# Optimization experiments

Hardware: AMD Instinct MI355X
Metric: run time of the kernel (lower is better)

## Reference

```python
import jax, jax.numpy as jnp
import numpy as np

LOG2 = np.float32(np.log(2.0))

def ssp(v):
    # shifted softplus used by SchNet
    return jax.nn.softplus(v) - LOG2

def setup_inputs() -> dict:
    key = jax.random.key(0)
    ks = jax.random.split(key, 12)
    B, A, T = 2, 512, 512          # batch, atoms, triplet-neighbors
    n_in, n_f, n_out, n_rbf = 128, 128, 128, 25
    x = jax.random.normal(ks[0], (B, A, n_in), dtype=jnp.float32)
    r_ij = jax.random.uniform(ks[1], (B, A, T, n_rbf), dtype=jnp.float32)
    pairwise_mask = jnp.ones((B, A, T), dtype=jnp.float32)
    neighbors_j = jax.random.randint(ks[2], (B, A, T), 0, A)
    neighbors_k = jax.random.randint(ks[3], (B, A, T), 0, A)
    s = 1.0 / np.sqrt(n_f)
    Wf1 = jax.random.normal(ks[4], (n_rbf, n_f), dtype=jnp.float32) / np.sqrt(n_rbf)
    bf1 = jnp.zeros((n_f,), dtype=jnp.float32)
    Wf2 = jax.random.normal(ks[5], (n_f, n_f), dtype=jnp.float32) * s
    bf2 = jnp.zeros((n_f,), dtype=jnp.float32)
    Win = jax.random.normal(ks[6], (n_in, n_f), dtype=jnp.float32) / np.sqrt(n_in)
    Wout = jax.random.normal(ks[7], (n_f, n_out), dtype=jnp.float32) * s
    bout = jnp.zeros((n_out,), dtype=jnp.float32)
    return {"x": x, "r_ij": r_ij, "pairwise_mask": pairwise_mask,
            "Wf1": Wf1, "bf1": bf1, "Wf2": Wf2, "bf2": bf2,
            "Win": Win, "Wout": Wout, "bout": bout,
            "neighbors_j": neighbors_j, "neighbors_k": neighbors_k}

def reference(x, r_ij, pairwise_mask, Wf1, bf1, Wf2, bf2, Win, Wout, bout,
              neighbors_j, neighbors_k):
    # filter network: Dense(n_rbf,F, ssp) -> Dense(F,F)
    W = ssp(jnp.einsum('batr,rf->batf', r_ij, Wf1) + bf1)
    W = jnp.einsum('batf,fg->batg', W, Wf2) + bf2          # [B,A,T,F]
    # in2f (no bias)
    y = jnp.einsum('bai,if->baf', x, Win)                  # [B,A,F]
    # double gather over triplet indices j,k (per-batch gather on atom axis)
    gather = jax.vmap(lambda yb, idx: yb[idx])             # [A,F],[A,T]->[A,T,F]
    y_j = gather(y, neighbors_j)                           # [B,A,T,F]
    y_k = gather(y, neighbors_k)                           # [B,A,T,F]
    # triple product + masked sum over triplet axis
    y = jnp.sum(y_j * W * y_k * pairwise_mask[..., None], axis=2)  # [B,A,F]
    # f2out with shifted-softplus activation
    return ssp(jnp.einsum('baf,fo->bao', y, Wout) + bout)
```

## Files before the change

### kernel.cpp

```cpp
#include <hip/hip_runtime.h>
#include <hip/hip_bf16.h>

typedef unsigned short u16;
typedef __attribute__((ext_vector_type(8))) short short8;
typedef __bf16 bf16x8 __attribute__((ext_vector_type(8)));
typedef __attribute__((ext_vector_type(4))) float float4v;
typedef __attribute__((ext_vector_type(4))) int int4v;

#define BB 2
#define AA 512
#define TT 512
#define FF 128
#define NRBF 25

__device__ float g_y[BB * AA * FF];
__device__ int   g_dtype;


__device__ __forceinline__ float bf2f(u16 u) {
    unsigned int v = ((unsigned int)u) << 16;
    return __builtin_bit_cast(float, v);
}
__device__ __forceinline__ u16 f2bf(float f) {
    unsigned int u = __builtin_bit_cast(unsigned int, f);
    u += 0x7fffu + ((u >> 16) & 1u);
    return (u16)(u >> 16);
}
__device__ __forceinline__ void split2(float v, u16& h, u16& l) {
    h = f2bf(v);
    l = f2bf(v - bf2f(h));
}
template<bool F32>
__device__ __forceinline__ float loadf(const void* p, int i) {
    return F32 ? ((const float*)p)[i] : bf2f(((const u16*)p)[i]);
}
__device__ __forceinline__ float ssp(float v) {
    float a = fabsf(v);
    float e = __builtin_amdgcn_exp2f(a * -1.44269504088896f);
    float l = __builtin_amdgcn_logf(1.0f + e);
    return fmaxf(v, 0.0f) + fmaf(0.69314718055995f, l, -0.69314718055995f);
}
__device__ __forceinline__ float4v mfma16(short8 a, short8 b, float4v c) {
    return __builtin_amdgcn_mfma_f32_16x16x32_bf16(
        __builtin_bit_cast(bf16x8, a), __builtin_bit_cast(bf16x8, b), c, 0, 0, 0);
}

__global__ __launch_bounds__(64) void k_detect(const void* r_raw) {
    const u16* p = (const u16*)r_raw;
    const int l = threadIdx.x;
    int sign = 0, zeros = 0;
#pragma unroll
    for (int i = 0; i < 8; ++i) {
        u16 v = p[2 * (l * 8 + i)];
        sign  += (v >> 15);
        zeros += (v == 0);
    }
#pragma unroll
    for (int off = 1; off < 64; off <<= 1) {
        sign  += __shfl_xor(sign, off);
        zeros += __shfl_xor(zeros, off);
    }
    if (l == 0) g_dtype = (sign || zeros > 400) ? 1 : 0;
}

template<bool F32>
__global__ __launch_bounds__(128) void k_in2f(const void* __restrict__ x,
                                              const void* __restrict__ Win) {
    if (g_dtype != (F32 ? 1 : 0)) return;
    int ba = blockIdx.x;
    int o  = threadIdx.x;
    __shared__ float sx[FF];
    sx[o] = loadf<F32>(x, ba * FF + o);
    __syncthreads();
    float s = 0.f;
#pragma unroll 8
    for (int i = 0; i < FF; ++i)
        s = fmaf(sx[i], loadf<F32>(Win, i * FF + o), s);
    g_y[ba * FF + o] = s;
}

template<bool F32>
__global__ __launch_bounds__(256, 3) void k_main(
    const void* __restrict__ r_ij, const void* __restrict__ mask,
    const void* __restrict__ Wf1,  const void* __restrict__ bf1,
    const void* __restrict__ Wf2,  const void* __restrict__ bf2_,
    const void* __restrict__ Wout, const void* __restrict__ bout,
    const int* __restrict__ nbrj,  const int* __restrict__ nbrk,
    void* __restrict__ out)
{
    if (g_dtype != (F32 ? 1 : 0)) return;
    const int ba  = blockIdx.x;
    const int tid = threadIdx.x;
    const int w   = tid >> 6;
    const int l   = tid & 63;
    const int lm  = l & 15;
    const int lq  = l >> 4;

    __shared__ __align__(16) u16 sRh[2][16][40];
    __shared__ __align__(16) u16 sRl[2][16][40];
    __shared__ __align__(16) u16 sH1h[16][136];
    __shared__ __align__(16) u16 sH1l[16][136];
    __shared__ __align__(16) int   sJ[2][16];
    __shared__ __align__(16) int   sK[2][16];
    __shared__ __align__(16) float sM[2][16];
    __shared__ float sAcc[FF];

    short8 fWf1h[2], fWf1l[2];
    short8 fWf2h[4][2], fWf2l[4][2];
    float  bf1v[2], bf2v[2];
#pragma unroll
    for (int q = 0; q < 2; ++q) {
        const int n = 32 * w + 16 * q + lm;
        short8 vh, vl;
#pragma unroll
        for (int j = 0; j < 8; ++j) {
            const int k = lq * 8 + j;
            float wv = (k < NRBF) ? loadf<F32>(Wf1, k * FF + n) : 0.f;
            u16 h, lo; split2(wv, h, lo);
            vh[j] = (short)h; vl[j] = (short)lo;
        }
        fWf1h[q] = vh;
        if (F32) fWf1l[q] = vl;
        bf1v[q] = loadf<F32>(bf1, n);
        bf2v[q] = loadf<F32>(bf2_, n);
#pragma unroll
        for (int kk = 0; kk < 4; ++kk) {
            short8 uh, ul;
#pragma unroll
            for (int j = 0; j < 8; ++j) {
                float wv = loadf<F32>(Wf2, (kk * 32 + lq * 8 + j) * FF + n);
                u16 h, lo; split2(wv, h, lo);
                uh[j] = (short)h; ul[j] = (short)lo;
            }
            fWf2h[kk][q] = uh;
            if (F32) fWf2l[kk][q] = ul;
        }
    }

    const float* yb = g_y + (ba >> 9) * (AA * FF);
    const float4v zero = {0.f, 0.f, 0.f, 0.f};
    float acc[2] = {0.f, 0.f};

    const int tt0 = tid >> 5,          k0 = tid & 31;
    const int tt1 = (tid + 256) >> 5,  k1 = tid & 31;

    {
        float v0 = (k0 < NRBF) ? loadf<F32>(r_ij, (ba * TT + tt0) * NRBF + k0) : 0.f;
        float v1 = (k1 < NRBF) ? loadf<F32>(r_ij, (ba * TT + tt1) * NRBF + k1) : 0.f;
        u16 h, lo;
        split2(v0, h, lo); sRh[0][tt0][k0] = h; if (F32) sRl[0][tt0][k0] = lo;
        split2(v1, h, lo); sRh[0][tt1][k1] = h; if (F32) sRl[0][tt1][k1] = lo;
        if (tid < 16) {
            sJ[0][tid] = nbrj[ba * TT + tid] & (AA - 1);
            sK[0][tid] = nbrk[ba * TT + tid] & (AA - 1);
            sM[0][tid] = loadf<F32>(mask, ba * TT + tid);
        }
    }

    for (int tile = 0; tile < TT / 16; ++tile) {
        const int b = tile & 1;
        __syncthreads();

        const int4v  Jv = *(const int4v*) &sJ[b][lq * 4];
        const int4v  Kv = *(const int4v*) &sK[b][lq * 4];
        const float4v Mv = *(const float4v*)&sM[b][lq * 4];
        float yjr[2][4], ykr[2][4];
#pragma unroll
        for (int q = 0; q < 2; ++q) {
            const int n = 32 * w + 16 * q + lm;
#pragma unroll
            for (int r = 0; r < 4; ++r) {
                yjr[q][r] = yb[Jv[r] * FF + n];
                ykr[q][r] = yb[Kv[r] * FF + n];
            }
        }

        float pre0 = 0.f, pre1 = 0.f, preM = 0.f;
        int   preJ = 0,   preK = 0;
        if (tile + 1 < TT / 16) {
            const int t0n = (tile + 1) * 16;
            if (k0 < NRBF)
                pre0 = loadf<F32>(r_ij, (ba * TT + t0n + tt0) * NRBF + k0);
            if (k1 < NRBF)
                pre1 = loadf<F32>(r_ij, (ba * TT + t0n + tt1) * NRBF + k1);
            if (tid < 16) {
                preJ = nbrj[ba * TT + t0n + tid];
                preK = nbrk[ba * TT + t0n + tid];
                preM = loadf<F32>(mask, ba * TT + t0n + tid);
            }
        }

        short8 aRh = *(const short8*)((const char*)&sRh[b][0][0] + lm * 80 + lq * 16);
        float4v c1[2];
        c1[0] = mfma16(aRh, fWf1h[0], zero);
        c1[1] = mfma16(aRh, fWf1h[1], zero);
        if (F32) {
            short8 aRl = *(const short8*)((const char*)&sRl[b][0][0] + lm * 80 + lq * 16);
            c1[0] = mfma16(aRl, fWf1h[0], c1[0]);
            c1[1] = mfma16(aRl, fWf1h[1], c1[1]);
            c1[0] = mfma16(aRh, fWf1l[0], c1[0]);
            c1[1] = mfma16(aRh, fWf1l[1], c1[1]);
        }
#pragma unroll
        for (int q = 0; q < 2; ++q) {
            const int n = 32 * w + 16 * q + lm;
#pragma unroll
            for (int r = 0; r < 4; ++r) {
                const int m = lq * 4 + r;
                float h1 = ssp(c1[q][r] + bf1v[q]);
                u16 h, lo; split2(h1, h, lo);
                sH1h[m][n] = h;
                sH1l[m][n] = lo;
            }
        }
        __syncthreads();

        float4v c2[2] = {zero, zero};
#pragma unroll
        for (int kk = 0; kk < 4; ++kk) {
            short8 aHh = *(const short8*)((const char*)&sH1h[0][0] + lm * 272 + kk * 64 + lq * 16);
            short8 aHl = *(const short8*)((const char*)&sH1l[0][0] + lm * 272 + kk * 64 + lq * 16);
            c2[0] = mfma16(aHh, fWf2h[kk][0], c2[0]);
            c2[1] = mfma16(aHh, fWf2h[kk][1], c2[1]);
            c2[0] = mfma16(aHl, fWf2h[kk][0], c2[0]);
            c2[1] = mfma16(aHl, fWf2h[kk][1], c2[1]);
            if (F32) {
                c2[0] = mfma16(aHh, fWf2l[kk][0], c2[0]);
                c2[1] = mfma16(aHh, fWf2l[kk][1], c2[1]);
            }
        }

#pragma unroll
        for (int q = 0; q < 2; ++q) {
            float a2 = 0.f;
#pragma unroll
            for (int r = 0; r < 4; ++r) {
                const float h2 = c2[q][r] + bf2v[q];
                a2 = fmaf(h2 * yjr[q][r], ykr[q][r] * Mv[r], a2);
            }
            acc[q] += a2;
        }

        if (tile + 1 < TT / 16) {
            const int bn = b ^ 1;
            u16 h, lo;
            split2(pre0, h, lo); sRh[bn][tt0][k0] = h; if (F32) sRl[bn][tt0][k0] = lo;
            split2(pre1, h, lo); sRh[bn][tt1][k1] = h; if (F32) sRl[bn][tt1][k1] = lo;
            if (tid < 16) {
                sJ[bn][tid] = preJ & (AA - 1);
                sK[bn][tid] = preK & (AA - 1);
                sM[bn][tid] = preM;
            }
        }
    }

#pragma unroll
    for (int q = 0; q < 2; ++q) {
        float v = acc[q];
        v += __shfl_xor(v, 16);
        v += __shfl_xor(v, 32);
        if (lq == 0) sAcc[32 * w + 16 * q + lm] = v;
    }
    __syncthreads();

    if (tid < FF) {
        float s = loadf<F32>(bout, tid);
#pragma unroll 8
        for (int f = 0; f < FF; ++f)
            s = fmaf(sAcc[f], loadf<F32>(Wout, f * FF + tid), s);
        const float r = ssp(s);
        if (F32) ((float*)out)[ba * FF + tid] = r;
        else     ((u16*)out)[ba * FF + tid]   = f2bf(r);
    }
}

extern "C" void kernel_launch(void* const* d_in, const int* in_sizes, int n_in,
                              void* d_out, int out_size, void* d_ws, size_t ws_size,
                              hipStream_t stream) {
    const void* x    = d_in[0];
    const void* r_ij = d_in[1];
    const void* mask = d_in[2];
    const void* Wf1  = d_in[3];
    const void* bf1  = d_in[4];
    const void* Wf2  = d_in[5];
    const void* bf2  = d_in[6];
    const void* Win  = d_in[7];
    const void* Wout = d_in[8];
    const void* bout = d_in[9];
    const int* nj    = (const int*)d_in[10];
    const int* nk    = (const int*)d_in[11];
    (void)d_ws; (void)ws_size; (void)in_sizes; (void)n_in; (void)out_size;

    k_detect<<<1, 64, 0, stream>>>(r_ij);
    k_in2f<false><<<BB * AA, 128, 0, stream>>>(x, Win);
    k_in2f<true ><<<BB * AA, 128, 0, stream>>>(x, Win);
    k_main<false><<<BB * AA, 256, 0, stream>>>(r_ij, mask, Wf1, bf1, Wf2, bf2,
                                               Wout, bout, nj, nk, d_out);
    k_main<true ><<<BB * AA, 256, 0, stream>>>(r_ij, mask, Wf1, bf1, Wf2, bf2,
                                               Wout, bout, nj, nk, d_out);
}
```

Baseline: 235.0 us.

## Split triplet axis across two blocks per atom and reduce in separate output kernel

Each (batch, atom) row is now handled by two blocks, each covering half of the triplet axis, so the main kernel launches twice as many workgroups. Partial sums go to a global buffer. A new kernel adds the two halves and applies the Wout projection and shifted softplus. This aims to raise occupancy and load balance across the GPU's compute units. The cost is reloading the Wf1/Wf2 fragments in twice as many blocks, extra global traffic for partials, and two more kernel launches.

```diff
diff --git a/kernel.cpp b/kernel.cpp
--- a/kernel.cpp
+++ b/kernel.cpp
@@ -12,8 +12,10 @@
 #define TT 512
 #define FF 128
 #define NRBF 25
+#define NHALF 2
 
 __device__ float g_y[BB * AA * FF];
+__device__ float g_part[BB * AA * NHALF * FF];
 __device__ int   g_dtype;
 
 
@@ -84,17 +86,18 @@
     const void* __restrict__ r_ij, const void* __restrict__ mask,
     const void* __restrict__ Wf1,  const void* __restrict__ bf1,
     const void* __restrict__ Wf2,  const void* __restrict__ bf2_,
-    const void* __restrict__ Wout, const void* __restrict__ bout,
-    const int* __restrict__ nbrj,  const int* __restrict__ nbrk,
-    void* __restrict__ out)
+    const int* __restrict__ nbrj,  const int* __restrict__ nbrk)
 {
     if (g_dtype != (F32 ? 1 : 0)) return;
-    const int ba  = blockIdx.x;
+    const int ba   = blockIdx.x >> 1;
+    const int half = blockIdx.x & 1;
     const int tid = threadIdx.x;
     const int w   = tid >> 6;
     const int l   = tid & 63;
     const int lm  = l & 15;
     const int lq  = l >> 4;
+    const int rb  = ba * TT + half * (TT / NHALF);
+    const int NT  = TT / NHALF / 16;
 
     __shared__ __align__(16) u16 sRh[2][16][40];
     __shared__ __align__(16) u16 sRl[2][16][40];
@@ -103,7 +106,6 @@
     __shared__ __align__(16) int   sJ[2][16];
     __shared__ __align__(16) int   sK[2][16];
     __shared__ __align__(16) float sM[2][16];
-    __shared__ float sAcc[FF];
 
     short8 fWf1h[2], fWf1l[2];
     short8 fWf2h[4][2], fWf2l[4][2];
@@ -145,19 +147,19 @@
     const int tt1 = (tid + 256) >> 5,  k1 = tid & 31;
 
     {
-        float v0 = (k0 < NRBF) ? loadf<F32>(r_ij, (ba * TT + tt0) * NRBF + k0) : 0.f;
-        float v1 = (k1 < NRBF) ? loadf<F32>(r_ij, (ba * TT + tt1) * NRBF + k1) : 0.f;
+        float v0 = (k0 < NRBF) ? loadf<F32>(r_ij, (rb + tt0) * NRBF + k0) : 0.f;
+        float v1 = (k1 < NRBF) ? loadf<F32>(r_ij, (rb + tt1) * NRBF + k1) : 0.f;
         u16 h, lo;
         split2(v0, h, lo); sRh[0][tt0][k0] = h; if (F32) sRl[0][tt0][k0] = lo;
         split2(v1, h, lo); sRh[0][tt1][k1] = h; if (F32) sRl[0][tt1][k1] = lo;
         if (tid < 16) {
-            sJ[0][tid] = nbrj[ba * TT + tid] & (AA - 1);
-            sK[0][tid] = nbrk[ba * TT + tid] & (AA - 1);
-            sM[0][tid] = loadf<F32>(mask, ba * TT + tid);
-        }
-    }
-
-    for (int tile = 0; tile < TT / 16; ++tile) {
+            sJ[0][tid] = nbrj[rb + tid] & (AA - 1);
+            sK[0][tid] = nbrk[rb + tid] & (AA - 1);
+            sM[0][tid] = loadf<F32>(mask, rb + tid);
+        }
+    }
+
+    for (int tile = 0; tile < NT; ++tile) {
         const int b = tile & 1;
         __syncthreads();
 
@@ -177,16 +179,16 @@
 
         float pre0 = 0.f, pre1 = 0.f, preM = 0.f;
         int   preJ = 0,   preK = 0;
-        if (tile + 1 < TT / 16) {
-            const int t0n = (tile + 1) * 16;
+        if (tile + 1 < NT) {
+            const int t0n = rb + (tile + 1) * 16;
             if (k0 < NRBF)
-                pre0 = loadf<F32>(r_ij, (ba * TT + t0n + tt0) * NRBF + k0);
+                pre0 = loadf<F32>(r_ij, (t0n + tt0) * NRBF + k0);
             if (k1 < NRBF)
-                pre1 = loadf<F32>(r_ij, (ba * TT + t0n + tt1) * NRBF + k1);
+                pre1 = loadf<F32>(r_ij, (t0n + tt1) * NRBF + k1);
             if (tid < 16) {
-                preJ = nbrj[ba * TT + t0n + tid];
-                preK = nbrk[ba * TT + t0n + tid];
-                preM = loadf<F32>(mask, ba * TT + t0n + tid);
+                preJ = nbrj[t0n + tid];
+                preK = nbrk[t0n + tid];
+                preM = loadf<F32>(mask, t0n + tid);
             }
         }
 
@@ -241,7 +243,7 @@
             acc[q] += a2;
         }
 
-        if (tile + 1 < TT / 16) {
+        if (tile + 1 < NT) {
             const int bn = b ^ 1;
             u16 h, lo;
             split2(pre0, h, lo); sRh[bn][tt0][k0] = h; if (F32) sRl[bn][tt0][k0] = lo;
@@ -259,19 +261,28 @@
         float v = acc[q];
         v += __shfl_xor(v, 16);
         v += __shfl_xor(v, 32);
-        if (lq == 0) sAcc[32 * w + 16 * q + lm] = v;
-    }
+        if (lq == 0)
+            g_part[(ba * NHALF + half) * FF + 32 * w + 16 * q + lm] = v;
+    }
+}
+
+template<bool F32>
+__global__ __launch_bounds__(128) void k_out(const void* __restrict__ Wout,
+                                             const void* __restrict__ bout,
+                                             void* __restrict__ out) {
+    if (g_dtype != (F32 ? 1 : 0)) return;
+    const int ba = blockIdx.x;
+    const int o  = threadIdx.x;
+    __shared__ float sA[FF];
+    sA[o] = g_part[(ba * NHALF + 0) * FF + o] + g_part[(ba * NHALF + 1) * FF + o];
     __syncthreads();
-
-    if (tid < FF) {
-        float s = loadf<F32>(bout, tid);
+    float s = loadf<F32>(bout, o);
 #pragma unroll 8
-        for (int f = 0; f < FF; ++f)
-            s = fmaf(sAcc[f], loadf<F32>(Wout, f * FF + tid), s);
-        const float r = ssp(s);
-        if (F32) ((float*)out)[ba * FF + tid] = r;
-        else     ((u16*)out)[ba * FF + tid]   = f2bf(r);
-    }
+    for (int f = 0; f < FF; ++f)
+        s = fmaf(sA[f], loadf<F32>(Wout, f * FF + o), s);
+    const float r = ssp(s);
+    if (F32) ((float*)out)[ba * FF + o] = r;
+    else     ((u16*)out)[ba * FF + o]   = f2bf(r);
 }
 
 extern "C" void kernel_launch(void* const* d_in, const int* in_sizes, int n_in,
@@ -294,8 +305,10 @@
     k_detect<<<1, 64, 0, stream>>>(r_ij);
     k_in2f<false><<<BB * AA, 128, 0, stream>>>(x, Win);
     k_in2f<true ><<<BB * AA, 128, 0, stream>>>(x, Win);
-    k_main<false><<<BB * AA, 256, 0, stream>>>(r_ij, mask, Wf1, bf1, Wf2, bf2,
-                                               Wout, bout, nj, nk, d_out);
-    k_main<true ><<<BB * AA, 256, 0, stream>>>(r_ij, mask, Wf1, bf1, Wf2, bf2,
-                                               Wout, bout, nj, nk, d_out);
-}
+    k_main<false><<<BB * AA * NHALF, 256, 0, stream>>>(r_ij, mask, Wf1, bf1,
+                                                       Wf2, bf2, nj, nk);
+    k_main<true ><<<BB * AA * NHALF, 256, 0, stream>>>(r_ij, mask, Wf1, bf1,
+                                                       Wf2, bf2, nj, nk);
+    k_out<false><<<BB * AA, 128, 0, stream>>>(Wout, bout, d_out);
+    k_out<true ><<<BB * AA, 128, 0, stream>>>(Wout, bout, d_out);
+}
```

New measurement: 229.5 us. 2.4% less time.
